# Kernel tuning notes

Hardware: AMD Instinct MI355X
Metric: run time of the kernel (lower is better)

The kernel has to match this reference:

```python
import jax, jax.numpy as jnp
import numpy as np
from jax import lax

NUM_CLASSES = 80
IOU_THR = 0.5
SCORE_THR = 0.5
MAX_BOXES = 100
NEG = jnp.float32(-1e9)


def setup_inputs() -> dict:
    key = jax.random.key(0)
    ks = jax.random.split(key, 9)
    B = 64
    d = {}
    d['bbox13'] = jax.random.uniform(ks[0], (B, 13, 13, 3, 4), dtype=jnp.float32)
    d['p13'] = jax.random.uniform(ks[1], (B, 13, 13, 3, 1), dtype=jnp.float32)
    d['c13'] = jax.random.uniform(ks[2], (B, 13, 13, 3, NUM_CLASSES), dtype=jnp.float32)
    d['bbox26'] = jax.random.uniform(ks[3], (B, 26, 26, 3, 4), dtype=jnp.float32)
    d['p26'] = jax.random.uniform(ks[4], (B, 26, 26, 3, 1), dtype=jnp.float32)
    d['c26'] = jax.random.uniform(ks[5], (B, 26, 26, 3, NUM_CLASSES), dtype=jnp.float32)
    d['bbox52'] = jax.random.uniform(ks[6], (B, 52, 52, 3, 4), dtype=jnp.float32)
    d['p52'] = jax.random.uniform(ks[7], (B, 52, 52, 3, 1), dtype=jnp.float32)
    d['c52'] = jax.random.uniform(ks[8], (B, 52, 52, 3, NUM_CLASSES), dtype=jnp.float32)
    return d


def _nms_single(boxes, scores):
    # boxes: [N, 4] as [y1, x1, y2, x2] (normalized internally like TF), scores: [N]
    y1 = jnp.minimum(boxes[:, 0], boxes[:, 2])
    y2 = jnp.maximum(boxes[:, 0], boxes[:, 2])
    x1 = jnp.minimum(boxes[:, 1], boxes[:, 3])
    x2 = jnp.maximum(boxes[:, 1], boxes[:, 3])
    area = (y2 - y1) * (x2 - x1)
    s0 = jnp.where(scores > SCORE_THR, scores, NEG)

    def step(s, _):
        i = jnp.argmax(s)
        sc = s[i]
        valid = sc > SCORE_THR
        iy1 = jnp.maximum(y1, y1[i]); iy2 = jnp.minimum(y2, y2[i])
        ix1 = jnp.maximum(x1, x1[i]); ix2 = jnp.minimum(x2, x2[i])
        inter = jnp.maximum(iy2 - iy1, 0.0) * jnp.maximum(ix2 - ix1, 0.0)
        union = area + area[i] - inter
        iou = jnp.where(union > 0, inter / union, 0.0)
        s = jnp.where(iou > IOU_THR, NEG, s).at[i].set(NEG)
        return s, (i, sc, valid)

    _, (idx, sel_s, valid) = lax.scan(step, s0, None, length=MAX_BOXES)
    b = jnp.clip(boxes[idx], 0.0, 1.0)          # TF combined NMS: clip_boxes=True
    b = jnp.where(valid[:, None], b, 0.0)       # pad invalid with zeros
    sel_s = jnp.where(valid, sel_s, 0.0)
    cls = jnp.zeros_like(sel_s)                 # single score class -> class id 0
    return b, sel_s, cls, valid.sum().astype(jnp.int32)


def reference(bbox13, p13, c13, bbox26, p26, c26, bbox52, p52, c52):
    B = bbox13.shape[0]
    nc = c13.shape[-1]
    bbox = jnp.concatenate([bbox13.reshape(B, -1, 4), bbox26.reshape(B, -1, 4), bbox52.reshape(B, -1, 4)], axis=1)
    p = jnp.concatenate([p13.reshape(B, -1), p26.reshape(B, -1), p52.reshape(B, -1)], axis=1)
    c = jnp.concatenate([c13.reshape(B, -1, nc), c26.reshape(B, -1, nc), c52.reshape(B, -1, nc)], axis=1)
    cls_idx = jnp.argmax(c, axis=-1).astype(jnp.float32)  # quirky: class *index* scales objectness
    score = p * cls_idx                                     # [B, N]
    b, s, cl, valid = jax.vmap(_nms_single)(bbox, score)
    pred = jnp.concatenate([b, s[..., None], cl[..., None]], axis=-1)  # [B, MAX_BOXES, 6]
    return pred, valid
```

## Files before the change

kernel.cpp:

```cpp
#include <hip/hip_runtime.h>

#define NUM_CLASSES 80
#define N13 507
#define N26 2028
#define N52 8112
#define NANCH (N13 + N26 + N52)
#define BATCH 64
#define MAXB 100
#define NB 3720
#define BOFF 0xFC00u
#define KPT 11
#define TOPK 1024
#define LCAP 4096
#define LMASK (LCAP-1)
#define APB 64

typedef unsigned long long u64;

__global__ __launch_bounds__(256) void score_kernel(
    const float* __restrict__ c13, const float* __restrict__ p13,
    const float* __restrict__ c26, const float* __restrict__ p26,
    const float* __restrict__ c52, const float* __restrict__ p52,
    float* __restrict__ scores)
{
    int a   = blockIdx.x * APB + (threadIdx.x >> 2);
    int sub = threadIdx.x & 3;
    int b   = blockIdx.y;
    if (a >= NANCH) return;
    const float* cbase; const float* pbase;
    if (a < N13)            { cbase = c13 + ((size_t)b*N13 + a) * NUM_CLASSES;           pbase = p13 + (size_t)b*N13 + a; }
    else if (a < N13+N26)   { cbase = c26 + ((size_t)b*N26 + (a-N13)) * NUM_CLASSES;     pbase = p26 + (size_t)b*N26 + (a-N13); }
    else                    { cbase = c52 + ((size_t)b*N52 + (a-N13-N26)) * NUM_CLASSES; pbase = p52 + (size_t)b*N52 + (a-N13-N26); }
    float mx = -1.0f; int mi = 0;
    #pragma unroll
    for (int q = 0; q < 5; ++q) {
        float4 v = *(const float4*)(cbase + q*16 + sub*4);
        int cb = q*16 + sub*4;
        if (v.x > mx) { mx = v.x; mi = cb+0; }
        if (v.y > mx) { mx = v.y; mi = cb+1; }
        if (v.z > mx) { mx = v.z; mi = cb+2; }
        if (v.w > mx) { mx = v.w; mi = cb+3; }
    }
    #pragma unroll
    for (int off = 1; off < 4; off <<= 1) {
        float ov = __shfl_xor(mx, off);
        int   oi = __shfl_xor(mi, off);
        if (ov > mx || (ov == mx && oi < mi)) { mx = ov; mi = oi; }
    }
    if (sub == 0) scores[(size_t)b*NANCH + a] = pbase[0] * (float)mi;
}

__device__ __forceinline__ float4 load_box(const float* __restrict__ b13,
                                           const float* __restrict__ b26,
                                           const float* __restrict__ b52,
                                           int b, int n)
{
    if (n < N13)          return *(const float4*)(b13 + ((size_t)b*N13 + n)*4);
    else if (n < N13+N26) return *(const float4*)(b26 + ((size_t)b*N26 + (n-N13))*4);
    else                  return *(const float4*)(b52 + ((size_t)b*N52 + (n-N13-N26))*4);
}

__global__ __launch_bounds__(1024) void nms_sort_scan(
    const float* __restrict__ scores,
    const float* __restrict__ b13, const float* __restrict__ b26, const float* __restrict__ b52,
    float* __restrict__ out)
{
    const int b    = blockIdx.x;
    const int tid  = threadIdx.x;
    const int lane = tid & 63;
    const int wid  = tid >> 6;

    __shared__ u64 lst[LCAP];
    __shared__ unsigned int cnt[NB];
    __shared__ unsigned int wtot[16];
    __shared__ float4 acc4[MAXB];
    __shared__ u64 sup_lds[16];
    __shared__ float outrec[MAXB][6];
    __shared__ int accN_s, T_s, L_s;

    const float* sc = scores + (size_t)b * NANCH;

    float sreg[KPT];
    #pragma unroll
    for (int k = 0; k < KPT; ++k) {
        int n = tid + (k << 10);
        sreg[k] = (n < NANCH) ? sc[n] : 0.f;
    }

    for (int i = tid; i < NB; i += 1024) cnt[i] = 0u;
    if (tid == 0) accN_s = 0;
    __syncthreads();

    #pragma unroll
    for (int k = 0; k < KPT; ++k) {
        float s = sreg[k];
        if (s > 0.5f) {
            unsigned int bk = (__float_as_uint(s) >> 14) - BOFF;
            if (bk >= NB) bk = NB - 1;
            atomicAdd(&cnt[bk], 1u);
        }
    }
    __syncthreads();

    unsigned int loc[4]; unsigned int s4 = 0u;
    #pragma unroll
    for (int q = 0; q < 4; ++q) {
        int r = tid*4 + q;
        unsigned int v = (r < NB) ? cnt[NB-1-r] : 0u;
        loc[q] = v; s4 += v;
    }
    unsigned int incl = s4;
    #pragma unroll
    for (int off = 1; off < 64; off <<= 1) {
        unsigned int v = __shfl_up(incl, off);
        if (lane >= off) incl += v;
    }
    if (lane == 63) wtot[wid] = incl;
    __syncthreads();
    unsigned int wexcl = 0u, total = 0u;
    #pragma unroll
    for (int w = 0; w < 16; ++w) { unsigned int t = wtot[w]; if (w < wid) wexcl += t; total += t; }
    unsigned int run = wexcl + (incl - s4);
    if (tid == 0) { T_s = 0; L_s = (int)total; }
    __syncthreads();
    #pragma unroll
    for (int q = 0; q < 4; ++q) {
        int r = tid*4 + q;
        if (r < NB) {
            int bk = NB-1-r;
            unsigned int c = loc[q];
            if (run < TOPK && run + c >= TOPK) { T_s = bk; L_s = (int)(run + c); }
            cnt[bk] = run;
            run += c;
        }
    }
    __syncthreads();
    const int total_i = (int)total;
    int Treg = T_s;
    int regionEnd = L_s;

    #pragma unroll
    for (int k = 0; k < KPT; ++k) {
        float s = sreg[k];
        if (s > 0.5f) {
            unsigned int bits = __float_as_uint(s);
            unsigned int bk = (bits >> 14) - BOFF;
            if (bk >= NB) bk = NB - 1;
            if ((int)bk >= Treg) {
                unsigned int pos = atomicAdd(&cnt[bk], 1u);
                lst[pos & LMASK] = ((u64)bits << 32) | (u64)(0xFFFFFFFFu - (unsigned int)(tid + (k<<10)));
            }
        }
    }
    __syncthreads();

    {
        u64 kk[4]; int tt[4];
        #pragma unroll
        for (int i = 0; i < 4; ++i) {
            int p = tid + (i << 10);
            tt[i] = -1; kk[i] = 0ull;
            if (p < regionEnd) {
                u64 key = lst[p & LMASK];
                unsigned int bk = (unsigned int)(key >> 46) - BOFF;
                if (bk >= NB) bk = NB - 1;
                unsigned int st = (bk+1 < NB) ? cnt[bk+1] : 0u;
                unsigned int e  = cnt[bk];
                unsigned int rank = 0u;
                for (unsigned int q = st; q < e; ++q) rank += (lst[q & LMASK] > key) ? 1u : 0u;
                kk[i] = key; tt[i] = (int)(st + rank);
            }
        }
        __syncthreads();
        #pragma unroll
        for (int i = 0; i < 4; ++i) if (tt[i] >= 0) lst[tt[i] & LMASK] = kk[i];
        __syncthreads();
    }

    int accN = 0;
    u64 key = 0ull; float4 bb = make_float4(0.f,0.f,0.f,0.f); float s = 0.f;
    if (lane < regionEnd) {
        key = lst[lane];
        unsigned int n = 0xFFFFFFFFu - (unsigned int)(key & 0xFFFFFFFFull);
        s = __uint_as_float((unsigned int)(key >> 32));
        bb = load_box(b13, b26, b52, b, (int)n);
    }

    int c = 0;
    while (c < total_i && accN < MAXB) {
        while (c + 64 > regionEnd && regionEnd < total_i) {
            int K2 = regionEnd + TOPK;
            if (tid == 0) { T_s = 0; L_s = total_i; }
            __syncthreads();
            for (int bk = tid; bk < Treg; bk += 1024) {
                unsigned int stv = cnt[bk];
                unsigned int ev  = (bk == 0) ? (unsigned int)total_i : cnt[bk-1];
                if (stv < (unsigned int)K2 && ev >= (unsigned int)K2) { T_s = bk; L_s = (int)ev; }
            }
            __syncthreads();
            int T2 = T_s, L2 = L_s;
            #pragma unroll
            for (int k = 0; k < KPT; ++k) {
                float sv = sreg[k];
                if (sv > 0.5f) {
                    unsigned int bits = __float_as_uint(sv);
                    int bk = (int)((bits >> 14) - BOFF);
                    if (bk >= NB) bk = NB - 1;
                    if (bk >= T2 && bk < Treg) {
                        unsigned int pos = atomicAdd(&cnt[bk], 1u);
                        lst[pos & LMASK] = ((u64)bits << 32) | (u64)(0xFFFFFFFFu - (unsigned int)(tid + (k<<10)));
                    }
                }
            }
            __syncthreads();
            {
                u64 kk[4]; int tt[4];
                #pragma unroll
                for (int i = 0; i < 4; ++i) {
                    int p = regionEnd + tid + (i << 10);
                    tt[i] = -1; kk[i] = 0ull;
                    if (p < L2) {
                        u64 k2 = lst[p & LMASK];
                        unsigned int bk = (unsigned int)(k2 >> 46) - BOFF;
                        if (bk >= NB) bk = NB - 1;
                        unsigned int st = (bk+1 < NB) ? cnt[bk+1] : 0u;
                        unsigned int e  = cnt[bk];
                        unsigned int rank = 0u;
                        for (unsigned int q = st; q < e; ++q) rank += (lst[q & LMASK] > k2) ? 1u : 0u;
                        kk[i] = k2; tt[i] = (int)(st + rank);
                    }
                }
                __syncthreads();
                #pragma unroll
                for (int i = 0; i < 4; ++i) if (tt[i] >= 0) lst[tt[i] & LMASK] = kk[i];
                __syncthreads();
            }
            Treg = T2; regionEnd = L2;
            key = 0ull; bb = make_float4(0.f,0.f,0.f,0.f); s = 0.f;
            if (c + lane < regionEnd) {
                key = lst[(c + lane) & LMASK];
                unsigned int n = 0xFFFFFFFFu - (unsigned int)(key & 0xFFFFFFFFull);
                s = __uint_as_float((unsigned int)(key >> 32));
                bb = load_box(b13, b26, b52, b, (int)n);
            }
        }

        int m = regionEnd - c; if (m > 64) m = 64;
        float oy1 = bb.x, ox1 = bb.y, oy2 = bb.z, ox2 = bb.w, cs = s;
        float y1 = fminf(oy1, oy2), y2 = fmaxf(oy1, oy2);
        float x1 = fminf(ox1, ox2), x2 = fmaxf(ox1, ox2);
        float ar = (y2-y1)*(x2-x1);

        int nc = c + 64;
        if (nc + lane < regionEnd) {
            key = lst[(nc + lane) & LMASK];
            unsigned int n = 0xFFFFFFFFu - (unsigned int)(key & 0xFFFFFFFFull);
            s = __uint_as_float((unsigned int)(key >> 32));
            bb = load_box(b13, b26, b52, b, (int)n);
        } else { s = 0.f; bb = make_float4(0.f,0.f,0.f,0.f); }

        bool supp = (lane >= m);
        #pragma unroll 2
        for (int j = wid; j < accN; j += 16) {
            float4 aj = acc4[j];
            float jar = (aj.z - aj.x) * (aj.w - aj.y);
            float iy1=fmaxf(y1,aj.x), iy2=fminf(y2,aj.z);
            float ix1=fmaxf(x1,aj.y), ix2=fminf(x2,aj.w);
            float inter=fmaxf(iy2-iy1,0.f)*fmaxf(ix2-ix1,0.f);
            float un=(ar+jar)-inter;
            supp |= (un > 0.f) && (inter/un > 0.5f);
        }
        u64 bal = __ballot(supp);
        if (lane == 0) sup_lds[wid] = bal;
        __syncthreads();

        if (wid == 0) {
            u64 B = 0ull;
            #pragma unroll
            for (int w = 0; w < 16; ++w) B |= sup_lds[w];
            u64 valid_m = (m >= 64) ? ~0ull : ((1ull << m) - 1ull);
            u64 rem = (~B) & valid_m;
            while (rem && accN < MAXB) {
                int j = __builtin_ctzll(rem);
                float jy1=__shfl(y1,j), jx1=__shfl(x1,j), jy2=__shfl(y2,j);
                float jx2=__shfl(x2,j), jar=__shfl(ar,j);
                if (lane == j) {
                    acc4[accN] = make_float4(y1, x1, y2, x2);
                    outrec[accN][0]=fminf(fmaxf(oy1,0.f),1.f);
                    outrec[accN][1]=fminf(fmaxf(ox1,0.f),1.f);
                    outrec[accN][2]=fminf(fmaxf(oy2,0.f),1.f);
                    outrec[accN][3]=fminf(fmaxf(ox2,0.f),1.f);
                    outrec[accN][4]=cs;
                    outrec[accN][5]=0.f;
                }
                float iy1=fmaxf(y1,jy1), iy2=fminf(y2,jy2);
                float ix1=fmaxf(x1,jx1), ix2=fminf(x2,jx2);
                float inter=fmaxf(iy2-iy1,0.f)*fmaxf(ix2-ix1,0.f);
                float un=(ar+jar)-inter;
                bool kill = (un > 0.f) && (inter/un > 0.5f);
                rem &= ~__ballot(kill);
                rem &= ~(1ull << j);
                accN++;
            }
            if (lane == 0) accN_s = accN;
        }
        __syncthreads();
        accN = accN_s;
        c += 64;
    }

    const int accNf = accN_s;
    float* outp = out + (size_t)b * (MAXB*6);
    for (int i = tid; i < MAXB*6; i += 1024) {
        int t = i / 6;
        outp[i] = (t < accNf) ? outrec[t][i % 6] : 0.f;
    }
    if (tid == 0) out[(size_t)BATCH*(MAXB*6) + b] = (float)accNf;
}

extern "C" void kernel_launch(void* const* d_in, const int* in_sizes, int n_in,
                              void* d_out, int out_size, void* d_ws, size_t ws_size,
                              hipStream_t stream)
{
    const float* bbox13 = (const float*)d_in[0];
    const float* p13    = (const float*)d_in[1];
    const float* c13    = (const float*)d_in[2];
    const float* bbox26 = (const float*)d_in[3];
    const float* p26    = (const float*)d_in[4];
    const float* c26    = (const float*)d_in[5];
    const float* bbox52 = (const float*)d_in[6];
    const float* p52    = (const float*)d_in[7];
    const float* c52    = (const float*)d_in[8];
    float* out    = (float*)d_out;
    float* scores = (float*)d_ws;

    dim3 g1((NANCH + APB - 1)/APB, BATCH);
    score_kernel<<<g1, 256, 0, stream>>>(c13, p13, c26, p26, c52, p52, scores);
    nms_sort_scan<<<BATCH, 1024, 0, stream>>>(scores, bbox13, bbox26, bbox52, out);
}
```

Before: 70.93 us.

## Precompute intra-chunk IoU matrix so greedy NMS walk uses readlane masks

Wave 0 now computes a 64x64 suppression bitmask over the current candidate chunk before the barrier, overlapping with the other waves' checks against accepted boxes. The serial greedy loop then only reads one lane's row mask per accepted box, replacing shuffles, IoU math, division and a ballot per iteration. Accepted boxes are written in parallel after the loop via popcount ranking. This adds up to 64 IoU evaluations per lane per chunk, even when few candidates survive.

New measurement: 69.95 us. About the same (-1.4%).

```diff
diff --git a/kernel.cpp b/kernel.cpp
--- a/kernel.cpp
+++ b/kernel.cpp
@@ -74,6 +74,7 @@
     __shared__ unsigned int cnt[NB];
     __shared__ unsigned int wtot[16];
     __shared__ float4 acc4[MAXB];
+    __shared__ float4 cbb[64];
     __shared__ u64 sup_lds[16];
     __shared__ float outrec[MAXB][6];
     __shared__ int accN_s, T_s, L_s;
@@ -272,6 +273,21 @@
         }
         u64 bal = __ballot(supp);
         if (lane == 0) sup_lds[wid] = bal;
+
+        u64 myrow = 0ull;
+        if (wid == 0) {
+            cbb[lane] = make_float4(y1, x1, y2, x2);
+            #pragma unroll 4
+            for (int k = 0; k < m; ++k) {
+                float4 ck = cbb[k];
+                float kar = (ck.z - ck.x) * (ck.w - ck.y);
+                float iy1=fmaxf(y1,ck.x), iy2=fminf(y2,ck.z);
+                float ix1=fmaxf(x1,ck.y), ix2=fminf(x2,ck.w);
+                float inter=fmaxf(iy2-iy1,0.f)*fmaxf(ix2-ix1,0.f);
+                float un=(ar+kar)-inter;
+                if ((un > 0.f) && (inter/un > 0.5f)) myrow |= (1ull << k);
+            }
+        }
         __syncthreads();
 
         if (wid == 0) {
@@ -280,27 +296,26 @@
             for (int w = 0; w < 16; ++w) B |= sup_lds[w];
             u64 valid_m = (m >= 64) ? ~0ull : ((1ull << m) - 1ull);
             u64 rem = (~B) & valid_m;
+            u64 accmask = 0ull;
+            const int start = accN;
             while (rem && accN < MAXB) {
                 int j = __builtin_ctzll(rem);
-                float jy1=__shfl(y1,j), jx1=__shfl(x1,j), jy2=__shfl(y2,j);
-                float jx2=__shfl(x2,j), jar=__shfl(ar,j);
-                if (lane == j) {
-                    acc4[accN] = make_float4(y1, x1, y2, x2);
-                    outrec[accN][0]=fminf(fmaxf(oy1,0.f),1.f);
-                    outrec[accN][1]=fminf(fmaxf(ox1,0.f),1.f);
-                    outrec[accN][2]=fminf(fmaxf(oy2,0.f),1.f);
-                    outrec[accN][3]=fminf(fmaxf(ox2,0.f),1.f);
-                    outrec[accN][4]=cs;
-                    outrec[accN][5]=0.f;
-                }
-                float iy1=fmaxf(y1,jy1), iy2=fminf(y2,jy2);
-                float ix1=fmaxf(x1,jx1), ix2=fminf(x2,jx2);
-                float inter=fmaxf(iy2-iy1,0.f)*fmaxf(ix2-ix1,0.f);
-                float un=(ar+jar)-inter;
-                bool kill = (un > 0.f) && (inter/un > 0.5f);
-                rem &= ~__ballot(kill);
+                u64 rowj = (u64)(unsigned int)__builtin_amdgcn_readlane((int)(myrow & 0xFFFFFFFFull), j)
+                         | ((u64)(unsigned int)__builtin_amdgcn_readlane((int)(myrow >> 32), j) << 32);
+                accmask |= (1ull << j);
+                rem &= ~rowj;
                 rem &= ~(1ull << j);
                 accN++;
+            }
+            if (accmask & (1ull << lane)) {
+                int pos = start + (int)__popcll(accmask & ((1ull << lane) - 1ull));
+                acc4[pos] = make_float4(y1, x1, y2, x2);
+                outrec[pos][0]=fminf(fmaxf(oy1,0.f),1.f);
+                outrec[pos][1]=fminf(fmaxf(ox1,0.f),1.f);
+                outrec[pos][2]=fminf(fmaxf(oy2,0.f),1.f);
+                outrec[pos][3]=fminf(fmaxf(ox2,0.f),1.f);
+                outrec[pos][4]=cs;
+                outrec[pos][5]=0.f;
             }
             if (lane == 0) accN_s = accN;
         }
```
